# Kernel tuning notes

Measured on AMD Instinct MI355X. Metric: run time of the kernel, lower is better.

## Reference

```python
import jax, jax.numpy as jnp
import numpy as np

N_USERS = 100000
N_ITEMS = 200000
N_NODES = N_USERS + N_ITEMS
NNZ = 3000000
DIM = 64
LM_DIM = 64
M_PHI = 1000
N_LAYERS = 3
SELECTED_K = 1000
BATCH = 8192


def _l2norm(x, eps=1e-12):
    return x / jnp.maximum(jnp.linalg.norm(x, axis=1, keepdims=True), eps)


def setup_inputs() -> dict:
    key = jax.random.key(0)
    ks = jax.random.split(key, 12)
    users = jax.random.randint(ks[0], (BATCH,), 0, N_USERS, dtype=jnp.int32)
    items = jax.random.randint(ks[1], (BATCH,), 0, N_ITEMS, dtype=jnp.int32)
    user_emb = 0.1 * jax.random.normal(ks[2], (N_USERS, DIM), jnp.float32)
    item_emb = 0.1 * jax.random.normal(ks[3], (N_ITEMS, DIM), jnp.float32)
    rows = jax.random.randint(ks[4], (NNZ,), 0, N_NODES, dtype=jnp.int32)
    cols = jax.random.randint(ks[5], (NNZ,), 0, N_NODES, dtype=jnp.int32)
    # normalized-adjacency-like values ~ 1/deg scale
    vals = jax.random.uniform(ks[6], (NNZ,), jnp.float32) * 0.1
    phi3 = jax.random.normal(ks[7], (N_USERS, DIM), jnp.float32) * 0.05
    phi4 = jax.random.normal(ks[8], (DIM, M_PHI), jnp.float32) * 0.05
    phi2 = jax.random.normal(ks[9], (N_USERS, M_PHI), jnp.float32) * 0.05
    # user_lm_T and item_lm are L2-normalized at module init
    user_lm_T = _l2norm(jax.random.normal(ks[10], (M_PHI, LM_DIM), jnp.float32))
    item_lm = _l2norm(jax.random.normal(ks[11], (N_ITEMS, LM_DIM), jnp.float32))
    return {"users": users, "items": items, "user_emb": user_emb,
            "item_emb": item_emb, "rows": rows, "cols": cols, "vals": vals,
            "phi3": phi3, "phi4": phi4, "phi2": phi2,
            "user_lm_T": user_lm_T, "item_lm": item_lm}


def _spmm(rows, cols, vals, x):
    # sparse (N,N) @ dense (N,D) via gather + segment_sum
    return jax.ops.segment_sum(vals[:, None] * x[cols], rows,
                               num_segments=N_NODES)


def reference(users, items, user_emb, item_emb, rows, cols, vals,
              phi3, phi4, phi2, user_lm_T, item_lm):
    # --- computer(): LightGCN propagation, mean over layers 0..L ---
    all_emb = jnp.concatenate([user_emb, item_emb], axis=0)  # [N, D]
    acc = all_emb
    e = all_emb
    for _ in range(N_LAYERS):
        e = _spmm(rows, cols, vals, e)
        acc = acc + e
    light_out = acc / (N_LAYERS + 1)
    users_id_emb = light_out[:N_USERS]
    items_id_emb = light_out[N_USERS:]

    # --- LM-side user embedding ---
    k = SELECTED_K
    phi1 = phi3 @ phi4                                   # [n_users, M]
    ulm_t = user_lm_T[:k]                                # [k, LM_DIM]
    user_lm = 0.1 * (phi1[:, :k] @ ulm_t) + 0.9 * (phi2[:, :k] @ ulm_t)

    # --- forward(users, items) ---
    gamma_id = jnp.sum(users_id_emb[users] * items_id_emb[items], axis=1)
    gamma_lm = jnp.sum(user_lm[users] * item_lm[items], axis=1)
    return 0.5 * gamma_id + gamma_lm
```

## Files before the change

kernel.cpp:

```cpp
#include <hip/hip_runtime.h>
#include <hip/hip_bf16.h>

#define N_USERS 100000
#define N_ITEMS 200000
#define N_NODES 300000
#define NNZ_    3000000
#define DIM     64
#define MPHI    1000
#define BATCH_  8192
#define TBROW   8

#define QSCALE  81920.0f
#define QINV    (1.0f / 81920.0f)
#define QMASK   8191u
#define CSHIFT  13

#define EMB_S   200.0f
#define E_S     512.0f
#define E_SI    (1.0f / 512.0f)

#define NBUCK   256
#define RPB     1172
#define BCAP    16384
#define EPT     8
#define EPW     (256 * EPT)
#define NBBIN   ((NNZ_ + EPW - 1) / EPW)
#define NBCAT   ((N_NODES * 16) / 256)
#define NB_SP   (N_NODES / 4)
#define NB_W2   (BATCH_ / TBROW)
#define NB_MARK 64

typedef unsigned int   uint32;

__device__ __forceinline__ int q8(float x) {
  int v = __float2int_rn(x);
  return v > 127 ? 127 : (v < -127 ? -127 : v);
}

__device__ __forceinline__ float row_dot_i8(int beg, int end,
                                            const uint32* __restrict__ cvs,
                                            const char* __restrict__ src,
                                            int lane) {
  float acc = 0.f;
  for (int e = beg; e < end; e += 16) {
    uint32 p[16];
    float  x[16];
#pragma unroll
    for (int k = 0; k < 16; k++) p[k] = (e + k < end) ? cvs[e + k] : 0u;
#pragma unroll
    for (int k = 0; k < 16; k++)
      x[k] = (float)src[(size_t)(p[k] >> CSHIFT) * DIM + lane];
#pragma unroll
    for (int k = 0; k < 16; k++)
      acc = fmaf((float)(p[k] & QMASK), x[k], acc);
  }
  return acc;
}

__global__ __launch_bounds__(256) void fusedA_k(const float* __restrict__ phi4,
                                                const float* __restrict__ ulm_t,
                                                float* __restrict__ W,
                                                const int* __restrict__ rows,
                                                const int* __restrict__ cols,
                                                const float* __restrict__ vals,
                                                int* __restrict__ bucket_fill,
                                                uint32* __restrict__ rcv,
                                                unsigned short* __restrict__ rloc,
                                                const float4* __restrict__ uemb,
                                                const float4* __restrict__ iemb,
                                                char4* __restrict__ emb8) {
  __shared__ int lh[NBUCK];
  __shared__ int lbase[NBUCK];
  __shared__ float part[4][64];
  int t = threadIdx.x;

  if (blockIdx.x < 64) {
    int d = blockIdx.x;
    int lane = t & 63, w = t >> 6;
    float s = 0.f;
    int k0 = w * 250, k1 = k0 + 250;
    for (int k = k0; k < k1; k++)
      s = fmaf(phi4[(size_t)d * MPHI + k], ulm_t[(size_t)k * DIM + lane], s);
    part[w][lane] = s;
    __syncthreads();
    if (w == 0)
      W[d * DIM + lane] = part[0][lane] + part[1][lane] + part[2][lane] + part[3][lane];
    return;
  }
  if (blockIdx.x >= 64 + NBBIN) {
    int i = (blockIdx.x - 64 - NBBIN) * 256 + t;
    const int NU4 = N_USERS * 16;
    float4 v = (i < NU4) ? uemb[i] : iemb[i - NU4];
    char4 o;
    o.x = (char)q8(v.x * EMB_S);
    o.y = (char)q8(v.y * EMB_S);
    o.z = (char)q8(v.z * EMB_S);
    o.w = (char)q8(v.w * EMB_S);
    emb8[i] = o;
    return;
  }
  int base = (blockIdx.x - 64) * EPW;
  lh[t] = 0;
  __syncthreads();

  int    vloc[EPT];
  uint32 vx[EPT];
  int    vrank[EPT];
  int    vbuck[EPT];
#pragma unroll
  for (int k = 0; k < EPT; k++) {
    int e = base + t + k * 256;
    bool ok = (e < NNZ_);
    int r = 0, c = 0;
    float v = 0.f;
    if (ok) { r = rows[e]; c = cols[e]; v = vals[e]; }
    int q = (int)(v * QSCALE + 0.5f);
    q = (q > 8191) ? 8191 : q;
    int b = r / RPB;
    vloc[k]  = r - b * RPB;
    vx[k]    = ((uint32)c << CSHIFT) | (uint32)q;
    vbuck[k] = b;
    vrank[k] = ok ? atomicAdd(&lh[b], 1) : -1;
  }
  __syncthreads();
  lbase[t] = (lh[t] > 0) ? atomicAdd(&bucket_fill[t], lh[t]) : 0;
  __syncthreads();
#pragma unroll
  for (int k = 0; k < EPT; k++) {
    if (vrank[k] >= 0) {
      int b = vbuck[k];
      int idx = b * BCAP + lbase[b] + vrank[k];
      rcv[idx]  = vx[k];
      rloc[idx] = (unsigned short)vloc[k];
    }
  }
}

__global__ __launch_bounds__(1024) void place3_k(const uint32* __restrict__ rcv,
                                                 const unsigned short* __restrict__ rloc,
                                                 const int* __restrict__ bucket_fill,
                                                 int2* __restrict__ rp2,
                                                 uint32* __restrict__ cvs,
                                                 int* __restrict__ needed) {
  __shared__ int sA[2048];
  __shared__ int sB[2048];
  __shared__ int off[RPB];
  int buck  = blockIdx.x;
  int base  = buck * BCAP;
  int rbase = buck * RPB;
  int n = bucket_fill[buck];
  int t = threadIdx.x;
  sA[t] = 0; sA[t + 1024] = 0;
  __syncthreads();
  const unsigned short* rl = rloc + base;
  for (int i = t; i < n; i += 1024) atomicAdd(&sA[rl[i]], 1);
  __syncthreads();
  int* s_ = sA;
  int* d_ = sB;
  for (int ofs = 1; ofs < 2048; ofs <<= 1) {
    for (int i = t; i < 2048; i += 1024)
      d_[i] = s_[i] + ((i >= ofs) ? s_[i - ofs] : 0);
    __syncthreads();
    int* tm = s_; s_ = d_; d_ = tm;
  }
  for (int i = t; i < RPB; i += 1024) {
    int r = rbase + i;
    if (r < N_NODES) {
      int b = (i == 0) ? 0 : s_[i - 1];
      rp2[r] = make_int2(base + b, base + s_[i]);
      off[i] = b;
      needed[r] = 0;
    }
  }
  __syncthreads();
  const uint32* rc = rcv + base;
  for (int i = t; i < n; i += 1024) {
    int pos = atomicAdd(&off[rl[i]], 1);
    cvs[base + pos] = rc[i];
  }
}

__global__ __launch_bounds__(256, 8) void fusedC_k(const int* __restrict__ users,
                                                   const int* __restrict__ items,
                                                   const int2* __restrict__ rp2,
                                                   const uint32* __restrict__ cvs,
                                                   const char* __restrict__ src,
                                                   char* __restrict__ dst,
                                                   float mult,
                                                   int* __restrict__ needed) {
  if (blockIdx.x < NB_MARK) {
    int w = blockIdx.x * 256 + threadIdx.x;
    int node = (w < BATCH_) ? users[w] : N_USERS + items[w - BATCH_];
    needed[node] = 1;
    int2 be = rp2[node];
    for (int e = be.x; e < be.y; e++)
      needed[cvs[e] >> CSHIFT] = 1;
    return;
  }
  int r = __builtin_amdgcn_readfirstlane((blockIdx.x - NB_MARK) * 4 + (threadIdx.x >> 6));
  int lane = threadIdx.x & 63;
  int2 be = rp2[r];
  float raw = row_dot_i8(be.x, be.y, cvs, src, lane);
  dst[(size_t)r * DIM + lane] = (char)q8(raw * mult);
}

__global__ __launch_bounds__(256, 8) void fusedD_k(const int* __restrict__ users,
                                                   const float* __restrict__ phi2,
                                                   const float* __restrict__ phi3,
                                                   const float* __restrict__ ulm_t,
                                                   const float* __restrict__ W,
                                                   float* __restrict__ wlm,
                                                   const int2* __restrict__ rp2,
                                                   const uint32* __restrict__ cvs,
                                                   const char* __restrict__ src,
                                                   const int* __restrict__ needed,
                                                   char* __restrict__ dst,
                                                   float mult) {
  __shared__ float u_s[64][68];
  __shared__ float p_s[TBROW][68];
  if (blockIdx.x < NB_W2) {
    int tid = threadIdx.x;
    int j = tid & 63;
    int g = tid >> 6;
    int b0 = blockIdx.x * TBROW;

    float acc[2] = {0.f, 0.f};
    for (int chunk = 0; chunk < 17; chunk++) {
      int kc = chunk * 64;
      bool lm = (chunk == 16);
      for (int idx = tid; idx < 64 * 16; idx += 256) {
        int kk = idx >> 4, c4 = (idx & 15) << 2;
        float4 v = make_float4(0.f, 0.f, 0.f, 0.f);
        if (lm) v = *(const float4*)(W + (size_t)kk * DIM + c4);
        else if (kc + kk < MPHI) v = *(const float4*)(ulm_t + (size_t)(kc + kk) * DIM + c4);
        *(float4*)&u_s[kk][c4] = v;
      }
      for (int idx = tid; idx < TBROW * 16; idx += 256) {
        int row = idx >> 4, c4 = (idx & 15) << 2;
        int u = users[b0 + row];
        float4 v = make_float4(0.f, 0.f, 0.f, 0.f);
        if (lm) {
          v = *(const float4*)(phi3 + (size_t)u * DIM + c4);
          v.x *= 0.1f; v.y *= 0.1f; v.z *= 0.1f; v.w *= 0.1f;
        } else if (kc + c4 < MPHI) {
          v = *(const float4*)(phi2 + (size_t)u * MPHI + kc + c4);
          v.x *= 0.9f; v.y *= 0.9f; v.z *= 0.9f; v.w *= 0.9f;
        }
        *(float4*)&p_s[row][c4] = v;
      }
      __syncthreads();
#pragma unroll
      for (int kk = 0; kk < 64; kk += 4) {
        float u0 = u_s[kk + 0][j];
        float u1 = u_s[kk + 1][j];
        float u2 = u_s[kk + 2][j];
        float u3 = u_s[kk + 3][j];
#pragma unroll
        for (int i = 0; i < 2; i++) {
          float4 p = *(const float4*)&p_s[g * 2 + i][kk];
          acc[i] = fmaf(p.w, u3, fmaf(p.z, u2, fmaf(p.y, u1, fmaf(p.x, u0, acc[i]))));
        }
      }
      __syncthreads();
    }
#pragma unroll
    for (int i = 0; i < 2; i++)
      wlm[(size_t)(b0 + g * 2 + i) * DIM + j] = acc[i];
    return;
  }
  int r = __builtin_amdgcn_readfirstlane((blockIdx.x - NB_W2) * 4 + (threadIdx.x >> 6));
  if (!needed[r]) return;
  int lane = threadIdx.x & 63;
  int2 be = rp2[r];
  float raw = row_dot_i8(be.x, be.y, cvs, src, lane);
  dst[(size_t)r * DIM + lane] = (char)q8(raw * mult);
}

__global__ __launch_bounds__(256, 8) void spmm_sel2_k(const int* __restrict__ users,
                                                      const int* __restrict__ items,
                                                      const int2* __restrict__ rp2,
                                                      const uint32* __restrict__ cvs,
                                                      const char* __restrict__ e1,
                                                      const char* __restrict__ e2,
                                                      const float* __restrict__ uemb,
                                                      const float* __restrict__ iemb,
                                                      float* __restrict__ acc_sel) {
  int w = blockIdx.x * 4 + (threadIdx.x >> 6);
  int lane = threadIdx.x & 63;
  int node = (w < BATCH_) ? users[w] : N_USERS + items[w - BATCH_];
  node = __builtin_amdgcn_readfirstlane(node);
  int2 be = rp2[node];
  float raw = row_dot_i8(be.x, be.y, cvs, e2, lane);
  float emb = (node < N_USERS)
                  ? uemb[(size_t)node * DIM + lane]
                  : iemb[(size_t)(node - N_USERS) * DIM + lane];
  float e1v = (float)e1[(size_t)node * DIM + lane] * E_SI;
  float e2v = (float)e2[(size_t)node * DIM + lane] * E_SI;
  acc_sel[(size_t)w * DIM + lane] = emb + e1v + e2v + raw * (QINV * E_SI);
}

__global__ __launch_bounds__(256) void final2_k(const int* __restrict__ items,
                                                const float* __restrict__ acc_sel,
                                                const float* __restrict__ wlm,
                                                const float* __restrict__ item_lm,
                                                float* __restrict__ out) {
  int tid = threadIdx.x;
  int wave = tid >> 6, lane = tid & 63;
  int b = blockIdx.x * 4 + wave;
  int it = items[b];
  float au = acc_sel[(size_t)b * DIM + lane];
  float ai = acc_sel[(size_t)(BATCH_ + b) * DIM + lane];
  float val = au * ai * (0.5f / 16.0f) +
              wlm[(size_t)b * DIM + lane] * item_lm[(size_t)it * DIM + lane];
#pragma unroll
  for (int o = 32; o > 0; o >>= 1) val += __shfl_xor(val, o, 64);
  if (lane == 0) out[b] = val;
}

__global__ __launch_bounds__(256) void compute_W_fb_k(const float* __restrict__ phi4,
                                                      const float* __restrict__ ulm_t,
                                                      float* __restrict__ W) {
  __shared__ float part[4][64];
  int d = blockIdx.x;
  int lane = threadIdx.x & 63, w = threadIdx.x >> 6;
  float s = 0.f;
  int k0 = w * 250, k1 = k0 + 250;
  for (int k = k0; k < k1; k++)
    s = fmaf(phi4[(size_t)d * MPHI + k], ulm_t[(size_t)k * DIM + lane], s);
  part[w][lane] = s;
  __syncthreads();
  if (w == 0)
    W[d * DIM + lane] = part[0][lane] + part[1][lane] + part[2][lane] + part[3][lane];
}

__global__ __launch_bounds__(256) void spmm_first_k(const int* __restrict__ rows,
                                                    const int* __restrict__ cols,
                                                    const float* __restrict__ vals,
                                                    const float* __restrict__ uemb,
                                                    const float* __restrict__ iemb,
                                                    float* __restrict__ dst) {
  int t = blockIdx.x * 256 + threadIdx.x;
  int e = t >> 4;
  if (e >= NNZ_) return;
  int sub = (t & 15) * 4;
  int c = cols[e];
  int r = rows[e];
  float v = vals[e];
  const float* src = (c < N_USERS) ? (uemb + (size_t)c * DIM)
                                   : (iemb + (size_t)(c - N_USERS) * DIM);
  float4 x = *(const float4*)(src + sub);
  float* d = dst + (size_t)r * DIM + sub;
  unsafeAtomicAdd(d + 0, v * x.x);
  unsafeAtomicAdd(d + 1, v * x.y);
  unsafeAtomicAdd(d + 2, v * x.z);
  unsafeAtomicAdd(d + 3, v * x.w);
}

__global__ __launch_bounds__(256) void spmm_k(const int* __restrict__ rows,
                                              const int* __restrict__ cols,
                                              const float* __restrict__ vals,
                                              const float* __restrict__ src,
                                              float* __restrict__ dst) {
  int t = blockIdx.x * 256 + threadIdx.x;
  int e = t >> 4;
  if (e >= NNZ_) return;
  int sub = (t & 15) * 4;
  int c = cols[e];
  int r = rows[e];
  float v = vals[e];
  float4 x = *(const float4*)(src + (size_t)c * DIM + sub);
  float* d = dst + (size_t)r * DIM + sub;
  unsafeAtomicAdd(d + 0, v * x.x);
  unsafeAtomicAdd(d + 1, v * x.y);
  unsafeAtomicAdd(d + 2, v * x.z);
  unsafeAtomicAdd(d + 3, v * x.w);
}

__global__ __launch_bounds__(256) void init_acc_k(const int* __restrict__ users,
                                                  const int* __restrict__ items,
                                                  const float* __restrict__ uemb,
                                                  const float* __restrict__ iemb,
                                                  const float* __restrict__ e1,
                                                  float* __restrict__ acc_sel) {
  int t = blockIdx.x * 256 + threadIdx.x;
  int b = t >> 6, j = t & 63;
  size_t node;
  float base;
  if (b < BATCH_) {
    int u = users[b];
    node = (size_t)u;
    base = uemb[(size_t)u * DIM + j];
  } else {
    int it = items[b - BATCH_];
    node = (size_t)(N_USERS + it);
    base = iemb[(size_t)it * DIM + j];
  }
  acc_sel[t] = base + e1[node * DIM + j];
}

__global__ __launch_bounds__(256) void gather_add_f32_k(const int* __restrict__ users,
                                                        const int* __restrict__ items,
                                                        const float* __restrict__ e,
                                                        float* __restrict__ acc_sel) {
  int t = blockIdx.x * 256 + threadIdx.x;
  int b = t >> 6, j = t & 63;
  size_t node = (b < BATCH_) ? (size_t)users[b] : (size_t)(N_USERS + items[b - BATCH_]);
  acc_sel[t] += e[node * DIM + j];
}

__global__ __launch_bounds__(256) void final_k(const int* __restrict__ users,
                                               const int* __restrict__ items,
                                               const float* __restrict__ acc_sel,
                                               const float* __restrict__ phi3,
                                               const float* __restrict__ phi2,
                                               const float* __restrict__ ulm_t,
                                               const float* __restrict__ item_lm,
                                               const float* __restrict__ W,
                                               float* __restrict__ out) {
  __shared__ float Ws[DIM * DIM];
  int tid = threadIdx.x;
  for (int i = tid; i < DIM * DIM; i += 256) Ws[i] = W[i];
  __syncthreads();
  int wave = tid >> 6, lane = tid & 63;
  int b = blockIdx.x * 4 + wave;
  if (b >= BATCH_) return;
  int u = users[b], it = items[b];
  float au = acc_sel[(size_t)b * DIM + lane];
  float ai = acc_sel[(size_t)(BATCH_ + b) * DIM + lane];
  float gid = au * ai * (1.0f / 16.0f);
  const float* p3 = phi3 + (size_t)u * DIM;
  float w3 = 0.f;
#pragma unroll
  for (int d2 = 0; d2 < DIM; d2++) w3 += p3[d2] * Ws[d2 * DIM + lane];
  const float* p2 = phi2 + (size_t)u * MPHI;
  float w2 = 0.f;
  for (int k = 0; k < MPHI; k += 4) {
    float4 p = *(const float4*)(p2 + k);
    w2 += p.x * ulm_t[(k + 0) * DIM + lane];
    w2 += p.y * ulm_t[(k + 1) * DIM + lane];
    w2 += p.z * ulm_t[(k + 2) * DIM + lane];
    w2 += p.w * ulm_t[(k + 3) * DIM + lane];
  }
  float il = item_lm[(size_t)it * DIM + lane];
  float val = gid * 0.5f + (0.1f * w3 + 0.9f * w2) * il;
#pragma unroll
  for (int o = 32; o > 0; o >>= 1) val += __shfl_xor(val, o, 64);
  if (lane == 0) out[b] = val;
}

extern "C" void kernel_launch(void* const* d_in, const int* in_sizes, int n_in,
                              void* d_out, int out_size, void* d_ws, size_t ws_size,
                              hipStream_t stream) {
  const int*   users    = (const int*)d_in[0];
  const int*   items    = (const int*)d_in[1];
  const float* user_emb = (const float*)d_in[2];
  const float* item_emb = (const float*)d_in[3];
  const int*   rows     = (const int*)d_in[4];
  const int*   cols     = (const int*)d_in[5];
  const float* vals     = (const float*)d_in[6];
  const float* phi3     = (const float*)d_in[7];
  const float* phi4     = (const float*)d_in[8];
  const float* phi2     = (const float*)d_in[9];
  const float* ulm_t    = (const float*)d_in[10];
  const float* item_lm  = (const float*)d_in[11];
  float* out = (float*)d_out;

  size_t o = 0;
  auto take = [&](size_t bytes) { size_t cur = o; o = (o + bytes + 255) & ~(size_t)255; return cur; };
  size_t off_buf0 = take((size_t)N_NODES * DIM);
  size_t off_buf1 = take((size_t)N_NODES * DIM);
  size_t off_wlm  = take((size_t)BATCH_ * DIM * 4);
  size_t off_acc  = take((size_t)2 * BATCH_ * DIM * 4);
  size_t off_W    = take((size_t)DIM * DIM * 4);
  size_t off_rp2  = take((size_t)(NBUCK * RPB + 8) * 8);
  size_t off_need = take((size_t)N_NODES * 4);
  size_t off_cvs  = take((size_t)NBUCK * BCAP * 4);
  size_t off_bfil = take((size_t)NBUCK * 4);
  size_t off_rcv  = take((size_t)NBUCK * BCAP * 4);
  size_t off_rloc = take((size_t)NBUCK * BCAP * 2);
  size_t need = o;

  char* base = (char*)d_ws;
  int selGrid = (2 * BATCH_ * DIM) / 256;

  size_t need_fb = 2 * ((size_t)N_NODES * DIM * 4) + (size_t)2 * BATCH_ * DIM * 4 + DIM * DIM * 4 + 4096;

  if (ws_size >= need) {
    char*  buf0    = (char*)(base + off_buf0);
    char*  buf1    = (char*)(base + off_buf1);
    float* wlm     = (float*)(base + off_wlm);
    float* acc_sel = (float*)(base + off_acc);
    float* W       = (float*)(base + off_W);
    int2*  rp2     = (int2*)(base + off_rp2);
    int*   needed  = (int*)(base + off_need);
    uint32* cvs    = (uint32*)(base + off_cvs);
    int*   bfill   = (int*)(base + off_bfil);
    uint32* rcv    = (uint32*)(base + off_rcv);
    unsigned short* rloc = (unsigned short*)(base + off_rloc);

    hipMemsetAsync(bfill, 0, (size_t)NBUCK * 4, stream);
    fusedA_k<<<64 + NBBIN + NBCAT, 256, 0, stream>>>(phi4, ulm_t, W,
                                                     rows, cols, vals,
                                                     bfill, rcv, rloc,
                                                     (const float4*)user_emb,
                                                     (const float4*)item_emb,
                                                     (char4*)buf0);
    place3_k<<<NBUCK, 1024, 0, stream>>>(rcv, rloc, bfill, rp2, cvs, needed);
    fusedC_k<<<NB_MARK + NB_SP, 256, 0, stream>>>(users, items, rp2, cvs,
                                                  buf0, buf1,
                                                  QINV * (E_S / EMB_S), needed);
    fusedD_k<<<NB_W2 + NB_SP, 256, 0, stream>>>(users, phi2, phi3, ulm_t, W, wlm,
                                                rp2, cvs, buf1, needed, buf0,
                                                QINV);
    spmm_sel2_k<<<(2 * BATCH_) / 4, 256, 0, stream>>>(users, items, rp2, cvs,
                                                      buf1, buf0,
                                                      user_emb, item_emb, acc_sel);
    final2_k<<<BATCH_ / 4, 256, 0, stream>>>(items, acc_sel, wlm, item_lm, out);
  } else if (ws_size >= need_fb) {
    float* buf0    = (float*)d_ws;
    float* buf1    = buf0 + (size_t)N_NODES * DIM;
    float* acc_sel = buf1 + (size_t)N_NODES * DIM;
    float* W       = acc_sel + (size_t)2 * BATCH_ * DIM;

    size_t ebytes = (size_t)N_NODES * DIM * sizeof(float);
    int spmmGrid = (NNZ_ * 16 + 255) / 256;

    compute_W_fb_k<<<64, 256, 0, stream>>>(phi4, ulm_t, W);

    hipMemsetAsync(buf0, 0, ebytes, stream);
    spmm_first_k<<<spmmGrid, 256, 0, stream>>>(rows, cols, vals, user_emb, item_emb, buf0);
    init_acc_k<<<selGrid, 256, 0, stream>>>(users, items, user_emb, item_emb, buf0, acc_sel);

    hipMemsetAsync(buf1, 0, ebytes, stream);
    spmm_k<<<spmmGrid, 256, 0, stream>>>(rows, cols, vals, buf0, buf1);
    gather_add_f32_k<<<selGrid, 256, 0, stream>>>(users, items, buf1, acc_sel);

    hipMemsetAsync(buf0, 0, ebytes, stream);
    spmm_k<<<spmmGrid, 256, 0, stream>>>(rows, cols, vals, buf1, buf0);
    gather_add_f32_k<<<selGrid, 256, 0, stream>>>(users, items, buf0, acc_sel);

    final_k<<<BATCH_ / 4, 256, 0, stream>>>(users, items, acc_sel, phi3, phi2,
                                            ulm_t, item_lm, W, out);
  }
}
```

Before: 295.6 us.

## Move LM-side batch matmul into placement kernel and fuse final gather with scoring

The LM-side per-user projection (phi2/phi3 times ulm_t/W) moves out of the third-layer SpMM kernel and runs as extra 1024-thread blocks in the bucket placement kernel, each handling 32 batch rows. The layer-3 masked SpMM becomes its own kernel. The selected-row SpMM and the final dot-product kernel are merged into one kernel with one block per batch element. That block combines user and item rows in shared memory, which removes the acc_sel round-trip and one launch. The trade-off is larger blocks and higher shared-memory use in the placement kernel, which may lower its occupancy or lengthen its tail.

```diff
diff --git a/kernel.cpp b/kernel.cpp
--- a/kernel.cpp
+++ b/kernel.cpp
@@ -8,7 +8,6 @@
 #define DIM     64
 #define MPHI    1000
 #define BATCH_  8192
-#define TBROW   8
 
 #define QSCALE  81920.0f
 #define QINV    (1.0f / 81920.0f)
@@ -27,7 +26,7 @@
 #define NBBIN   ((NNZ_ + EPW - 1) / EPW)
 #define NBCAT   ((N_NODES * 16) / 256)
 #define NB_SP   (N_NODES / 4)
-#define NB_W2   (BATCH_ / TBROW)
+#define NB_W2   256
 #define NB_MARK 64
 
 typedef unsigned int   uint32;
@@ -136,20 +135,82 @@
   }
 }
 
-__global__ __launch_bounds__(1024) void place3_k(const uint32* __restrict__ rcv,
+__global__ __launch_bounds__(1024) void fusedB_k(const uint32* __restrict__ rcv,
                                                  const unsigned short* __restrict__ rloc,
                                                  const int* __restrict__ bucket_fill,
                                                  int2* __restrict__ rp2,
                                                  uint32* __restrict__ cvs,
-                                                 int* __restrict__ needed) {
+                                                 int* __restrict__ needed,
+                                                 const int* __restrict__ users,
+                                                 const float* __restrict__ phi2,
+                                                 const float* __restrict__ phi3,
+                                                 const float* __restrict__ ulm_t,
+                                                 const float* __restrict__ W,
+                                                 float* __restrict__ wlm) {
   __shared__ int sA[2048];
   __shared__ int sB[2048];
   __shared__ int off[RPB];
+  __shared__ float u_s[64][68];
+  __shared__ float p_s[4][8][68];
+  int t = threadIdx.x;
+
+  if (blockIdx.x >= NBUCK) {
+    int bid = blockIdx.x - NBUCK;
+    int sub = t >> 8;
+    int t2  = t & 255;
+    int j   = t2 & 63;
+    int g   = t2 >> 6;
+    int b0  = bid * 32 + sub * 8;
+
+    float acc[2] = {0.f, 0.f};
+    for (int chunk = 0; chunk < 17; chunk++) {
+      int kc = chunk * 64;
+      bool lm = (chunk == 16);
+      for (int idx = t; idx < 64 * 16; idx += 1024) {
+        int kk = idx >> 4, c4 = (idx & 15) << 2;
+        float4 v = make_float4(0.f, 0.f, 0.f, 0.f);
+        if (lm) v = *(const float4*)(W + (size_t)kk * DIM + c4);
+        else if (kc + kk < MPHI) v = *(const float4*)(ulm_t + (size_t)(kc + kk) * DIM + c4);
+        *(float4*)&u_s[kk][c4] = v;
+      }
+      for (int idx = t2; idx < 8 * 16; idx += 256) {
+        int row = idx >> 4, c4 = (idx & 15) << 2;
+        int u = users[b0 + row];
+        float4 v = make_float4(0.f, 0.f, 0.f, 0.f);
+        if (lm) {
+          v = *(const float4*)(phi3 + (size_t)u * DIM + c4);
+          v.x *= 0.1f; v.y *= 0.1f; v.z *= 0.1f; v.w *= 0.1f;
+        } else if (kc + c4 < MPHI) {
+          v = *(const float4*)(phi2 + (size_t)u * MPHI + kc + c4);
+          v.x *= 0.9f; v.y *= 0.9f; v.z *= 0.9f; v.w *= 0.9f;
+        }
+        *(float4*)&p_s[sub][row][c4] = v;
+      }
+      __syncthreads();
+#pragma unroll
+      for (int kk = 0; kk < 64; kk += 4) {
+        float u0 = u_s[kk + 0][j];
+        float u1 = u_s[kk + 1][j];
+        float u2 = u_s[kk + 2][j];
+        float u3 = u_s[kk + 3][j];
+#pragma unroll
+        for (int i = 0; i < 2; i++) {
+          float4 p = *(const float4*)&p_s[sub][g * 2 + i][kk];
+          acc[i] = fmaf(p.w, u3, fmaf(p.z, u2, fmaf(p.y, u1, fmaf(p.x, u0, acc[i]))));
+        }
+      }
+      __syncthreads();
+    }
+#pragma unroll
+    for (int i = 0; i < 2; i++)
+      wlm[(size_t)(b0 + g * 2 + i) * DIM + j] = acc[i];
+    return;
+  }
+
   int buck  = blockIdx.x;
   int base  = buck * BCAP;
   int rbase = buck * RPB;
   int n = bucket_fill[buck];
-  int t = threadIdx.x;
   sA[t] = 0; sA[t + 1024] = 0;
   __syncthreads();
   const unsigned short* rl = rloc + base;
@@ -204,71 +265,13 @@
   dst[(size_t)r * DIM + lane] = (char)q8(raw * mult);
 }
 
-__global__ __launch_bounds__(256, 8) void fusedD_k(const int* __restrict__ users,
-                                                   const float* __restrict__ phi2,
-                                                   const float* __restrict__ phi3,
-                                                   const float* __restrict__ ulm_t,
-                                                   const float* __restrict__ W,
-                                                   float* __restrict__ wlm,
-                                                   const int2* __restrict__ rp2,
-                                                   const uint32* __restrict__ cvs,
-                                                   const char* __restrict__ src,
-                                                   const int* __restrict__ needed,
-                                                   char* __restrict__ dst,
-                                                   float mult) {
-  __shared__ float u_s[64][68];
-  __shared__ float p_s[TBROW][68];
-  if (blockIdx.x < NB_W2) {
-    int tid = threadIdx.x;
-    int j = tid & 63;
-    int g = tid >> 6;
-    int b0 = blockIdx.x * TBROW;
-
-    float acc[2] = {0.f, 0.f};
-    for (int chunk = 0; chunk < 17; chunk++) {
-      int kc = chunk * 64;
-      bool lm = (chunk == 16);
-      for (int idx = tid; idx < 64 * 16; idx += 256) {
-        int kk = idx >> 4, c4 = (idx & 15) << 2;
-        float4 v = make_float4(0.f, 0.f, 0.f, 0.f);
-        if (lm) v = *(const float4*)(W + (size_t)kk * DIM + c4);
-        else if (kc + kk < MPHI) v = *(const float4*)(ulm_t + (size_t)(kc + kk) * DIM + c4);
-        *(float4*)&u_s[kk][c4] = v;
-      }
-      for (int idx = tid; idx < TBROW * 16; idx += 256) {
-        int row = idx >> 4, c4 = (idx & 15) << 2;
-        int u = users[b0 + row];
-        float4 v = make_float4(0.f, 0.f, 0.f, 0.f);
-        if (lm) {
-          v = *(const float4*)(phi3 + (size_t)u * DIM + c4);
-          v.x *= 0.1f; v.y *= 0.1f; v.z *= 0.1f; v.w *= 0.1f;
-        } else if (kc + c4 < MPHI) {
-          v = *(const float4*)(phi2 + (size_t)u * MPHI + kc + c4);
-          v.x *= 0.9f; v.y *= 0.9f; v.z *= 0.9f; v.w *= 0.9f;
-        }
-        *(float4*)&p_s[row][c4] = v;
-      }
-      __syncthreads();
-#pragma unroll
-      for (int kk = 0; kk < 64; kk += 4) {
-        float u0 = u_s[kk + 0][j];
-        float u1 = u_s[kk + 1][j];
-        float u2 = u_s[kk + 2][j];
-        float u3 = u_s[kk + 3][j];
-#pragma unroll
-        for (int i = 0; i < 2; i++) {
-          float4 p = *(const float4*)&p_s[g * 2 + i][kk];
-          acc[i] = fmaf(p.w, u3, fmaf(p.z, u2, fmaf(p.y, u1, fmaf(p.x, u0, acc[i]))));
-        }
-      }
-      __syncthreads();
-    }
-#pragma unroll
-    for (int i = 0; i < 2; i++)
-      wlm[(size_t)(b0 + g * 2 + i) * DIM + j] = acc[i];
-    return;
-  }
-  int r = __builtin_amdgcn_readfirstlane((blockIdx.x - NB_W2) * 4 + (threadIdx.x >> 6));
+__global__ __launch_bounds__(256, 8) void spmm_csr_masked_k(const int2* __restrict__ rp2,
+                                                            const uint32* __restrict__ cvs,
+                                                            const char* __restrict__ src,
+                                                            const int* __restrict__ needed,
+                                                            char* __restrict__ dst,
+                                                            float mult) {
+  int r = __builtin_amdgcn_readfirstlane(blockIdx.x * 4 + (threadIdx.x >> 6));
   if (!needed[r]) return;
   int lane = threadIdx.x & 63;
   int2 be = rp2[r];
@@ -276,18 +279,21 @@
   dst[(size_t)r * DIM + lane] = (char)q8(raw * mult);
 }
 
-__global__ __launch_bounds__(256, 8) void spmm_sel2_k(const int* __restrict__ users,
-                                                      const int* __restrict__ items,
-                                                      const int2* __restrict__ rp2,
-                                                      const uint32* __restrict__ cvs,
-                                                      const char* __restrict__ e1,
-                                                      const char* __restrict__ e2,
-                                                      const float* __restrict__ uemb,
-                                                      const float* __restrict__ iemb,
-                                                      float* __restrict__ acc_sel) {
-  int w = blockIdx.x * 4 + (threadIdx.x >> 6);
-  int lane = threadIdx.x & 63;
-  int node = (w < BATCH_) ? users[w] : N_USERS + items[w - BATCH_];
+__global__ __launch_bounds__(128) void fusedEF_k(const int* __restrict__ users,
+                                                 const int* __restrict__ items,
+                                                 const int2* __restrict__ rp2,
+                                                 const uint32* __restrict__ cvs,
+                                                 const char* __restrict__ e1,
+                                                 const char* __restrict__ e2,
+                                                 const float* __restrict__ uemb,
+                                                 const float* __restrict__ iemb,
+                                                 const float* __restrict__ wlm,
+                                                 const float* __restrict__ item_lm,
+                                                 float* __restrict__ out) {
+  __shared__ float accs[2][64];
+  int b = blockIdx.x;
+  int wave = threadIdx.x >> 6, lane = threadIdx.x & 63;
+  int node = (wave == 0) ? users[b] : N_USERS + items[b];
   node = __builtin_amdgcn_readfirstlane(node);
   int2 be = rp2[node];
   float raw = row_dot_i8(be.x, be.y, cvs, e2, lane);
@@ -296,25 +302,16 @@
                   : iemb[(size_t)(node - N_USERS) * DIM + lane];
   float e1v = (float)e1[(size_t)node * DIM + lane] * E_SI;
   float e2v = (float)e2[(size_t)node * DIM + lane] * E_SI;
-  acc_sel[(size_t)w * DIM + lane] = emb + e1v + e2v + raw * (QINV * E_SI);
-}
-
-__global__ __launch_bounds__(256) void final2_k(const int* __restrict__ items,
-                                                const float* __restrict__ acc_sel,
-                                                const float* __restrict__ wlm,
-                                                const float* __restrict__ item_lm,
-                                                float* __restrict__ out) {
-  int tid = threadIdx.x;
-  int wave = tid >> 6, lane = tid & 63;
-  int b = blockIdx.x * 4 + wave;
-  int it = items[b];
-  float au = acc_sel[(size_t)b * DIM + lane];
-  float ai = acc_sel[(size_t)(BATCH_ + b) * DIM + lane];
-  float val = au * ai * (0.5f / 16.0f) +
-              wlm[(size_t)b * DIM + lane] * item_lm[(size_t)it * DIM + lane];
-#pragma unroll
-  for (int o = 32; o > 0; o >>= 1) val += __shfl_xor(val, o, 64);
-  if (lane == 0) out[b] = val;
+  accs[wave][lane] = emb + e1v + e2v + raw * (QINV * E_SI);
+  __syncthreads();
+  if (wave == 0) {
+    int it = items[b];
+    float val = accs[0][lane] * accs[1][lane] * (0.5f / 16.0f) +
+                wlm[(size_t)b * DIM + lane] * item_lm[(size_t)it * DIM + lane];
+#pragma unroll
+    for (int o = 32; o > 0; o >>= 1) val += __shfl_xor(val, o, 64);
+    if (lane == 0) out[b] = val;
+  }
 }
 
 __global__ __launch_bounds__(256) void compute_W_fb_k(const float* __restrict__ phi4,
@@ -470,7 +467,6 @@
   size_t off_buf0 = take((size_t)N_NODES * DIM);
   size_t off_buf1 = take((size_t)N_NODES * DIM);
   size_t off_wlm  = take((size_t)BATCH_ * DIM * 4);
-  size_t off_acc  = take((size_t)2 * BATCH_ * DIM * 4);
   size_t off_W    = take((size_t)DIM * DIM * 4);
   size_t off_rp2  = take((size_t)(NBUCK * RPB + 8) * 8);
   size_t off_need = take((size_t)N_NODES * 4);
@@ -489,7 +485,6 @@
     char*  buf0    = (char*)(base + off_buf0);
     char*  buf1    = (char*)(base + off_buf1);
     float* wlm     = (float*)(base + off_wlm);
-    float* acc_sel = (float*)(base + off_acc);
     float* W       = (float*)(base + off_W);
     int2*  rp2     = (int2*)(base + off_rp2);
     int*   needed  = (int*)(base + off_need);
@@ -505,17 +500,14 @@
                                                      (const float4*)user_emb,
                                                      (const float4*)item_emb,
                                                      (char4*)buf0);
-    place3_k<<<NBUCK, 1024, 0, stream>>>(rcv, rloc, bfill, rp2, cvs, needed);
+    fusedB_k<<<NBUCK + NB_W2, 1024, 0, stream>>>(rcv, rloc, bfill, rp2, cvs, needed,
+                                                 users, phi2, phi3, ulm_t, W, wlm);
     fusedC_k<<<NB_MARK + NB_SP, 256, 0, stream>>>(users, items, rp2, cvs,
                                                   buf0, buf1,
                                                   QINV * (E_S / EMB_S), needed);
-    fusedD_k<<<NB_W2 + NB_SP, 256, 0, stream>>>(users, phi2, phi3, ulm_t, W, wlm,
-                                                rp2, cvs, buf1, needed, buf0,
-                                                QINV);
-    spmm_sel2_k<<<(2 * BATCH_) / 4, 256, 0, stream>>>(users, items, rp2, cvs,
-                                                      buf1, buf0,
-                                                      user_emb, item_emb, acc_sel);
-    final2_k<<<BATCH_ / 4, 256, 0, stream>>>(items, acc_sel, wlm, item_lm, out);
+    spmm_csr_masked_k<<<NB_SP, 256, 0, stream>>>(rp2, cvs, buf1, needed, buf0, QINV);
+    fusedEF_k<<<BATCH_, 128, 0, stream>>>(users, items, rp2, cvs, buf1, buf0,
+                                          user_emb, item_emb, wlm, item_lm, out);
   } else if (ws_size >= need_fb) {
     float* buf0    = (float*)d_ws;
     float* buf1    = buf0 + (size_t)N_NODES * DIM;
```

New measurement: 297.5 us. About the same (+0.6%).
